# Kernel optimization log

Measured on AMD Instinct MI355X. Metric: run time of the kernel, lower is better.

Reference implementation:

```python
import jax, jax.numpy as jnp
import numpy as np

N_HEAD = 16
D_MODEL = 1024

def setup_inputs() -> dict:
    key = jax.random.key(0)
    ks = jax.random.split(key, 9)
    B, S, D = 8, 1024, D_MODEL
    scale = 1.0 / np.sqrt(D)
    inp = {
        'q': jax.random.normal(ks[0], (B, S, D), jnp.float32),
        'k': jax.random.normal(ks[1], (B, S, D), jnp.float32),
        'v': jax.random.normal(ks[2], (B, S, D), jnp.float32),
        'w_q': jax.random.normal(ks[3], (D, D), jnp.float32) * scale,
        'b_q': jnp.zeros((D,), jnp.float32),
        'w_k': jax.random.normal(ks[4], (D, D), jnp.float32) * scale,
        'b_k': jnp.zeros((D,), jnp.float32),
        'w_v': jax.random.normal(ks[5], (D, D), jnp.float32) * scale,
        'b_v': jnp.zeros((D,), jnp.float32),
    }
    return inp

def reference(q, k, v, w_q, b_q, w_k, b_k, w_v, b_v):
    B, S, D = q.shape
    H = N_HEAD
    dk = D // H
    # QKV projections, split into heads: [B, S, D] -> [B, H, S, dk]
    def proj(x, w, b):
        return (x @ w + b).reshape(B, S, H, dk).transpose(0, 2, 1, 3)
    qh = proj(q, w_q, b_q)
    kh = proj(k, w_k, b_k)
    vh = proj(v, w_v, b_v)
    # scaled dot-product attention (attention matrix materialized as in source)
    scores = jnp.einsum('bhqd,bhkd->bhqk', qh, kh) / jnp.sqrt(jnp.asarray(dk, q.dtype))
    attn = jax.nn.softmax(scores, axis=-1)
    # dropout disabled (eval mode)
    out = jnp.einsum('bhqk,bhkd->bhqd', attn, vh)  # [B, H, S, dk]
    return out.transpose(0, 2, 1, 3).reshape(B, S, D)
```

## Files before the change

kernel.cpp:

```cpp
#include <hip/hip_runtime.h>
#include <hip/hip_bf16.h>

#define BB 8
#define SS 1024
#define DD 1024
#define HH 16
#define DK 64
#define MM (BB*SS)

typedef __attribute__((ext_vector_type(8))) short bf16x8;
typedef __attribute__((ext_vector_type(4))) short bf16x4;
typedef __attribute__((ext_vector_type(4))) float f32x4;
typedef __attribute__((ext_vector_type(4))) int i32x4;

#define QSCALE 0.18033688011112042f

static __device__ __forceinline__ short f2bf(float f) {
    union { float f; unsigned u; } x; x.f = f;
    unsigned r = x.u + 0x7fffu + ((x.u >> 16) & 1u);
    return (short)(r >> 16);
}

#define GLOAD16(g, s) __builtin_amdgcn_global_load_lds( \
    (const __attribute__((address_space(1))) void*)(g), \
    (__attribute__((address_space(3))) void*)(s), 16, 0, 0)

__global__ void wtrans_kernel(const float* __restrict__ w0, const float* __restrict__ w1,
                              const float* __restrict__ w2, short* __restrict__ wt) {
    __shared__ short t[32][33];
    int p = blockIdx.z;
    const float* wsrc = p == 0 ? w0 : (p == 1 ? w1 : w2);
    short* dst = wt + (size_t)p * DD * DD;
    int k0 = blockIdx.y * 32, n0 = blockIdx.x * 32;
    int tx = threadIdx.x & 31, ty = threadIdx.x >> 5;
    #pragma unroll
    for (int i = 0; i < 4; ++i) {
        int k = ty + 8 * i;
        t[k][tx] = f2bf(wsrc[(size_t)(k0 + k) * DD + n0 + tx]);
    }
    __syncthreads();
    #pragma unroll
    for (int i = 0; i < 4; ++i) {
        int n = ty + 8 * i;
        dst[(size_t)(n0 + n) * DD + k0 + tx] = t[tx][n];
    }
}

__global__ void xcast_kernel(const float* __restrict__ xq, const float* __restrict__ xk,
                             const float* __restrict__ xv, short* __restrict__ xbf) {
    int z = blockIdx.y;
    const float* src = z == 0 ? xq : (z == 1 ? xk : xv);
    size_t i = ((size_t)blockIdx.x * 256 + threadIdx.x) * 8;
    f32x4 a = *(const f32x4*)(src + i);
    f32x4 b = *(const f32x4*)(src + i + 4);
    bf16x8 pk;
    pk[0] = f2bf(a[0]); pk[1] = f2bf(a[1]); pk[2] = f2bf(a[2]); pk[3] = f2bf(a[3]);
    pk[4] = f2bf(b[0]); pk[5] = f2bf(b[1]); pk[6] = f2bf(b[2]); pk[7] = f2bf(b[3]);
    *(bf16x8*)(xbf + (size_t)z * MM * DD + i) = pk;
}

#define BM 128
#define BN 128
#define BK 64

template<int ABF16>
__launch_bounds__(256, 3)
__global__ void qkvproj_kernel(const float* __restrict__ xq, const float* __restrict__ xk,
                               const float* __restrict__ xv,
                               const short* __restrict__ xbf,
                               const short* __restrict__ wt,
                               const float* __restrict__ bq, const float* __restrict__ bk,
                               const float* __restrict__ bv,
                               short* __restrict__ qh, short* __restrict__ kh,
                               short* __restrict__ vh) {
    __shared__ short As[BM * 64];
    __shared__ short Bs[BN * 64];
    int lin = blockIdx.x + 8 * (blockIdx.y + 64 * blockIdx.z);
    int sz = (lin & 7) * 192 + (lin >> 3);
    int p = sz >> 9;
    int n0 = (sz & 7) * BN;
    int m0 = ((sz >> 3) & 63) * BM;
    const float* X = p == 0 ? xq : (p == 1 ? xk : xv);
    const short* Wt = wt + (size_t)p * DD * DD;
    const float* bias = p == 0 ? bq : (p == 1 ? bk : bv);
    short* out = p == 0 ? qh : (p == 1 ? kh : vh);
    int t = threadIdx.x;
    int l = t & 63, w = t >> 6;
    int wm = (w >> 1) * 64, wn = (w & 1) * 64;
    int lg = l >> 4, lr = l & 15;
    int rx = lr & 7;

    f32x4 acc[4][4];
    #pragma unroll
    for (int mi = 0; mi < 4; ++mi)
        #pragma unroll
        for (int ni = 0; ni < 4; ++ni) acc[mi][ni] = 0.f;

    for (int k0 = 0; k0 < DD; k0 += BK) {
        __syncthreads();
        if constexpr (ABF16) {
            const short* Xb = xbf + (size_t)p * MM * DD;
            #pragma unroll
            for (int j = 0; j < 4; ++j) {
                int chunk = j * 256 + t;
                int row = chunk >> 3, seg = chunk & 7;
                const short* src = Xb + (size_t)(m0 + row) * DD + k0 + ((seg ^ (row & 7)) * 8);
                GLOAD16(src, &As[(j * 256 + w * 64) * 8]);
            }
        } else {
            #pragma unroll
            for (int i = 0; i < 4; ++i) {
                int c = t + 256 * i;
                int row = c >> 3, seg = c & 7;
                const float* src = X + (size_t)(m0 + row) * DD + k0 + seg * 8;
                f32x4 f0 = *(const f32x4*)(src);
                f32x4 f1 = *(const f32x4*)(src + 4);
                bf16x8 pk;
                pk[0] = f2bf(f0[0]); pk[1] = f2bf(f0[1]); pk[2] = f2bf(f0[2]); pk[3] = f2bf(f0[3]);
                pk[4] = f2bf(f1[0]); pk[5] = f2bf(f1[1]); pk[6] = f2bf(f1[2]); pk[7] = f2bf(f1[3]);
                *(bf16x8*)(&As[row * 64 + ((seg ^ (row & 7)) * 8)]) = pk;
            }
        }
        #pragma unroll
        for (int j = 0; j < 4; ++j) {
            int chunk = j * 256 + t;
            int row = chunk >> 3, seg = chunk & 7;
            const short* src = Wt + (size_t)(n0 + row) * DD + k0 + ((seg ^ (row & 7)) * 8);
            GLOAD16(src, &Bs[(j * 256 + w * 64) * 8]);
        }
        __syncthreads();
        #pragma unroll
        for (int kk = 0; kk < 2; ++kk) {
            bf16x8 a[4], b[4];
            #pragma unroll
            for (int mi = 0; mi < 4; ++mi)
                a[mi] = *(const bf16x8*)(&As[(wm + mi * 16 + lr) * 64 + (((kk * 4 + lg) ^ rx) * 8)]);
            #pragma unroll
            for (int ni = 0; ni < 4; ++ni)
                b[ni] = *(const bf16x8*)(&Bs[(wn + ni * 16 + lr) * 64 + (((kk * 4 + lg) ^ rx) * 8)]);
            #pragma unroll
            for (int mi = 0; mi < 4; ++mi)
                #pragma unroll
                for (int ni = 0; ni < 4; ++ni)
                    acc[mi][ni] = __builtin_amdgcn_mfma_f32_16x16x32_bf16(a[mi], b[ni], acc[mi][ni], 0, 0, 0);
        }
    }
    float osc = (p == 0) ? QSCALE : 1.0f;
    #pragma unroll
    for (int ni = 0; ni < 4; ++ni) {
        int n = n0 + wn + ni * 16 + lr;
        float bvv = bias[n];
        int h = n >> 6, dd = n & 63;
        #pragma unroll
        for (int mi = 0; mi < 4; ++mi) {
            int mbase = m0 + wm + mi * 16 + lg * 4;
            #pragma unroll
            for (int r = 0; r < 4; ++r) {
                int m = mbase + r;
                int b_ = m >> 10, s_ = m & 1023;
                out[(((size_t)(b_ * HH + h) * SS + s_) * DK) + dd] = f2bf((acc[mi][ni][r] + bvv) * osc);
            }
        }
    }
}

__global__ void vtrans_kernel(const short* __restrict__ vh, short* __restrict__ vt) {
    __shared__ short tile[64 * 72];
    int bh = blockIdx.y;
    int s0 = blockIdx.x * 64;
    int t = threadIdx.x;
    #pragma unroll
    for (int i = 0; i < 2; ++i) {
        int c = t + 256 * i;
        int row = c >> 3, dc = (c & 7) * 8;
        *(bf16x8*)&tile[row * 72 + dc] =
            *(const bf16x8*)(vh + ((size_t)bh * SS + s0 + row) * DK + dc);
    }
    __syncthreads();
    #pragma unroll
    for (int i = 0; i < 2; ++i) {
        int c = t + 256 * i;
        int dr = c >> 3, scc = (c & 7) * 8;
        bf16x8 vv;
        #pragma unroll
        for (int j = 0; j < 8; ++j) vv[j] = tile[(scc + j) * 72 + dr];
        *(bf16x8*)(vt + ((size_t)bh * DK + dr) * SS + s0 + scc) = vv;
    }
}


#define SOFTMAX_PV(KT, VT, AQ0, AQ1, MQ, LQ, OO) {                          \
    f32x4 sc[4];                                                            \
    __builtin_amdgcn_s_setprio(1);                                          \
    _Pragma("unroll")                                                       \
    for (int ct = 0; ct < 4; ++ct) {                                        \
        int row = ct * 16 + lr;                                             \
        bf16x8 k0 = *(const bf16x8*)&KT[row * 64 + ((lg ^ sw) * 8)];        \
        bf16x8 k1 = *(const bf16x8*)&KT[row * 64 + (((lg + 4) ^ sw) * 8)];  \
        f32x4 z = 0.f;                                                      \
        z = __builtin_amdgcn_mfma_f32_16x16x32_bf16(k0, AQ0, z, 0, 0, 0);   \
        z = __builtin_amdgcn_mfma_f32_16x16x32_bf16(k1, AQ1, z, 0, 0, 0);   \
        sc[ct] = z;                                                         \
    }                                                                       \
    __builtin_amdgcn_s_setprio(0);                                          \
    float t0 = fmaxf(fmaxf(sc[0][0], sc[0][1]), fmaxf(sc[0][2], sc[0][3])); \
    float t1 = fmaxf(fmaxf(sc[1][0], sc[1][1]), fmaxf(sc[1][2], sc[1][3])); \
    float t2 = fmaxf(fmaxf(sc[2][0], sc[2][1]), fmaxf(sc[2][2], sc[2][3])); \
    float t3 = fmaxf(fmaxf(sc[3][0], sc[3][1]), fmaxf(sc[3][2], sc[3][3])); \
    float tm = fmaxf(fmaxf(t0, t1), fmaxf(t2, t3));                         \
    tm = fmaxf(tm, __shfl_xor(tm, 16, 64));                                 \
    tm = fmaxf(tm, __shfl_xor(tm, 32, 64));                                 \
    if (__any(tm > MQ + 8.0f)) {                                            \
        float mn = fmaxf(MQ, tm);                                           \
        float alpha = exp2f(MQ - mn);                                       \
        MQ = mn; LQ *= alpha;                                               \
        _Pragma("unroll")                                                   \
        for (int r = 0; r < 4; ++r) {                                       \
            float ar = __shfl(alpha, lg * 4 + r, 64);                       \
            OO[0][r] *= ar; OO[1][r] *= ar; OO[2][r] *= ar; OO[3][r] *= ar; \
        }                                                                   \
    }                                                                       \
    float p_[4][4];                                                         \
    _Pragma("unroll")                                                       \
    for (int ct = 0; ct < 4; ++ct) {                                        \
        p_[ct][0] = exp2f(sc[ct][0] - MQ);                                  \
        p_[ct][1] = exp2f(sc[ct][1] - MQ);                                  \
        p_[ct][2] = exp2f(sc[ct][2] - MQ);                                  \
        p_[ct][3] = exp2f(sc[ct][3] - MQ);                                  \
    }                                                                       \
    float rs = ((p_[0][0] + p_[0][1]) + (p_[0][2] + p_[0][3]))              \
             + ((p_[1][0] + p_[1][1]) + (p_[1][2] + p_[1][3]))              \
             + ((p_[2][0] + p_[2][1]) + (p_[2][2] + p_[2][3]))              \
             + ((p_[3][0] + p_[3][1]) + (p_[3][2] + p_[3][3]));             \
    rs += __shfl_xor(rs, 16, 64);                                           \
    rs += __shfl_xor(rs, 32, 64);                                           \
    LQ += rs;                                                               \
    unsigned X00, X01, X10, X11, X20, X21, X30, X31;                        \
    asm("v_cvt_pk_bf16_f32 %0, %1, %2" : "=v"(X00) : "v"(p_[0][0]), "v"(p_[0][1])); \
    asm("v_cvt_pk_bf16_f32 %0, %1, %2" : "=v"(X01) : "v"(p_[0][2]), "v"(p_[0][3])); \
    asm("v_cvt_pk_bf16_f32 %0, %1, %2" : "=v"(X10) : "v"(p_[1][0]), "v"(p_[1][1])); \
    asm("v_cvt_pk_bf16_f32 %0, %1, %2" : "=v"(X11) : "v"(p_[1][2]), "v"(p_[1][3])); \
    asm("v_cvt_pk_bf16_f32 %0, %1, %2" : "=v"(X20) : "v"(p_[2][0]), "v"(p_[2][1])); \
    asm("v_cvt_pk_bf16_f32 %0, %1, %2" : "=v"(X21) : "v"(p_[2][2]), "v"(p_[2][3])); \
    asm("v_cvt_pk_bf16_f32 %0, %1, %2" : "=v"(X30) : "v"(p_[3][0]), "v"(p_[3][1])); \
    asm("v_cvt_pk_bf16_f32 %0, %1, %2" : "=v"(X31) : "v"(p_[3][2]), "v"(p_[3][3])); \
    auto r0 = __builtin_amdgcn_permlane32_swap((int)X00, (int)X10, false, false); \
    auto r1 = __builtin_amdgcn_permlane32_swap((int)X01, (int)X11, false, false); \
    auto r2 = __builtin_amdgcn_permlane32_swap((int)X20, (int)X30, false, false); \
    auto r3 = __builtin_amdgcn_permlane32_swap((int)X21, (int)X31, false, false); \
    i32x4 pa0i = { (int)r0[0], (int)r1[0], (int)r0[1], (int)r1[1] };        \
    i32x4 pa1i = { (int)r2[0], (int)r3[0], (int)r2[1], (int)r3[1] };        \
    bf16x8 pa0 = __builtin_bit_cast(bf16x8, pa0i);                          \
    bf16x8 pa1 = __builtin_bit_cast(bf16x8, pa1i);                          \
    __builtin_amdgcn_s_setprio(1);                                          \
    _Pragma("unroll")                                                       \
    for (int dt = 0; dt < 4; ++dt) {                                        \
        int row = dt * 16 + lr;                                             \
        bf16x8 v0 = *(const bf16x8*)&VT[row * 64 + ((lg ^ sw) * 8)];        \
        bf16x8 v1 = *(const bf16x8*)&VT[row * 64 + (((lg + 4) ^ sw) * 8)];  \
        OO[dt] = __builtin_amdgcn_mfma_f32_16x16x32_bf16(pa0, v0, OO[dt], 0, 0, 0); \
        OO[dt] = __builtin_amdgcn_mfma_f32_16x16x32_bf16(pa1, v1, OO[dt], 0, 0, 0); \
    }                                                                       \
    __builtin_amdgcn_s_setprio(0);                                          \
}

__launch_bounds__(256, 4)
__global__ void attn_kernel(const short* __restrict__ qh, const short* __restrict__ kh,
                            const short* __restrict__ vt, float* __restrict__ out) {
    __shared__ short KBuf[2][64 * 64];
    __shared__ short VBuf[2][64 * 64];
    int lin = blockIdx.y * 8 + blockIdx.x;
    int swz = (lin & 7) * 128 + (lin >> 3);
    int bh = swz >> 3;
    int q0 = (swz & 7) * 128;
    int t = threadIdx.x, l = t & 63, w = t >> 6;
    int lg = l >> 4, lr = l & 15;
    int sw = lr & 7;
    const short* Q  = qh + (size_t)bh * SS * DK;
    const short* Kg = kh + (size_t)bh * SS * DK;
    const short* Vg = vt + (size_t)bh * DK * SS;

    int qrow = q0 + w * 32 + lr;
    bf16x8 aq00 = *(const bf16x8*)(Q + (size_t)qrow * DK + lg * 8);
    bf16x8 aq01 = *(const bf16x8*)(Q + (size_t)qrow * DK + 32 + lg * 8);
    bf16x8 aq10 = *(const bf16x8*)(Q + (size_t)(qrow + 16) * DK + lg * 8);
    bf16x8 aq11 = *(const bf16x8*)(Q + (size_t)(qrow + 16) * DK + 32 + lg * 8);

    float m_q0 = -1e30f, l_q0 = 0.f, m_q1 = -1e30f, l_q1 = 0.f;
    f32x4 o0[4], o1[4];
    #pragma unroll
    for (int dt = 0; dt < 4; ++dt) { o0[dt] = 0.f; o1[dt] = 0.f; }

#define STAGE_KV(kv, b) { \
    _Pragma("unroll") \
    for (int j = 0; j < 2; ++j) { \
        int c = (j * 4 + w) * 64 + l; \
        int row = c >> 3, s = c & 7; \
        int rowg = (row & ~12) | ((row & 4) << 1) | ((row & 8) >> 1); \
        GLOAD16(Kg + (size_t)((kv) + rowg) * DK + ((s ^ (row & 7)) * 8), \
                &KBuf[b][(j * 4 + w) * 512]); \
        GLOAD16(Vg + (size_t)row * SS + (kv) + ((s ^ (row & 7)) * 8), \
                &VBuf[b][(j * 4 + w) * 512]); \
    } }

    STAGE_KV(0, 0);
    __syncthreads();

    for (int tt = 0; tt < 16; ++tt) {
        int cur = tt & 1;
        if (tt < 15) STAGE_KV((tt + 1) * 64, cur ^ 1);
        const short* KT = &KBuf[cur][0];
        const short* VT = &VBuf[cur][0];
        SOFTMAX_PV(KT, VT, aq00, aq01, m_q0, l_q0, o0);
        SOFTMAX_PV(KT, VT, aq10, aq11, m_q1, l_q1, o1);
        __syncthreads();
    }
#undef STAGE_KV

    int b_ = bh >> 4, h_ = bh & 15;
    #pragma unroll
    for (int r = 0; r < 4; ++r) {
        float ls0 = __shfl(l_q0, lg * 4 + r, 64);
        float inv0 = 1.0f / ls0;
        int srow0 = q0 + w * 32 + lg * 4 + r;
        float* op0 = out + ((size_t)(b_ * SS + srow0)) * DD + h_ * DK;
        #pragma unroll
        for (int dt = 0; dt < 4; ++dt)
            op0[dt * 16 + lr] = o0[dt][r] * inv0;
        float ls1 = __shfl(l_q1, lg * 4 + r, 64);
        float inv1 = 1.0f / ls1;
        int srow1 = srow0 + 16;
        float* op1 = out + ((size_t)(b_ * SS + srow1)) * DD + h_ * DK;
        #pragma unroll
        for (int dt = 0; dt < 4; ++dt)
            op1[dt * 16 + lr] = o1[dt][r] * inv1;
    }
}

extern "C" void kernel_launch(void* const* d_in, const int* in_sizes, int n_in,
                              void* d_out, int out_size, void* d_ws, size_t ws_size,
                              hipStream_t stream) {
    const float* q  = (const float*)d_in[0];
    const float* k  = (const float*)d_in[1];
    const float* v  = (const float*)d_in[2];
    const float* wq = (const float*)d_in[3];
    const float* bq = (const float*)d_in[4];
    const float* wk = (const float*)d_in[5];
    const float* bk = (const float*)d_in[6];
    const float* wv = (const float*)d_in[7];
    const float* bv = (const float*)d_in[8];
    float* out = (float*)d_out;

    char* ws = (char*)d_ws;
    const size_t SZ = (size_t)BB * HH * SS * DK * sizeof(short);
    short* Qh = (short*)(ws);
    short* Kh = (short*)(ws + SZ);
    short* Vh = (short*)(ws + 2 * SZ);
    short* Vt = (short*)(ws + 3 * SZ);
    short* Wt = (short*)(ws + 4 * SZ);
    const size_t XOFF = 4 * SZ + 3 * (size_t)DD * DD * sizeof(short);
    short* Xbf = (short*)(ws + XOFF);
    const size_t need = XOFF + 3 * (size_t)MM * DD * sizeof(short);

    wtrans_kernel<<<dim3(32, 32, 3), 256, 0, stream>>>(wq, wk, wv, Wt);
    if (ws_size >= need) {
        xcast_kernel<<<dim3(MM * DD / (256 * 8), 3), 256, 0, stream>>>(q, k, v, Xbf);
        qkvproj_kernel<1><<<dim3(8, 64, 3), 256, 0, stream>>>(q, k, v, Xbf, Wt, bq, bk, bv, Qh, Kh, Vh);
    } else {
        qkvproj_kernel<0><<<dim3(8, 64, 3), 256, 0, stream>>>(q, k, v, nullptr, Wt, bq, bk, bv, Qh, Kh, Vh);
    }
    vtrans_kernel<<<dim3(16, 128), 256, 0, stream>>>(Vh, Vt);
    attn_kernel<<<dim3(8, 128), 256, 0, stream>>>(Qh, Kh, Vt, out);
}
```

Baseline: 155.3 us.

## Fuse fp32 cast into projection loads and compute softmax row sums via MFMA

Drops the separate xcast kernel and its bf16 workspace copy of the inputs. The projection GEMM now always reads fp32 activations and converts them to bf16 in registers before writing to LDS, which saves a full extra read and write pass over the inputs but loses the async global-to-LDS loads for A. In the attention kernel, the softmax row sum is no longer built from VALU adds and shuffles; an extra MFMA against a vector of ones accumulates it, and the max reduction uses v_max3_f32.

After: 164.1 us. 1.06x slower.

```diff
diff --git a/kernel.cpp b/kernel.cpp
--- a/kernel.cpp
+++ b/kernel.cpp
@@ -19,6 +19,12 @@
     union { float f; unsigned u; } x; x.f = f;
     unsigned r = x.u + 0x7fffu + ((x.u >> 16) & 1u);
     return (short)(r >> 16);
+}
+
+static __device__ __forceinline__ float max3f(float a, float b, float c) {
+    float d;
+    asm("v_max3_f32 %0, %1, %2, %3" : "=v"(d) : "v"(a), "v"(b), "v"(c));
+    return d;
 }
 
 #define GLOAD16(g, s) __builtin_amdgcn_global_load_lds( \
@@ -46,28 +52,13 @@
     }
 }
 
-__global__ void xcast_kernel(const float* __restrict__ xq, const float* __restrict__ xk,
-                             const float* __restrict__ xv, short* __restrict__ xbf) {
-    int z = blockIdx.y;
-    const float* src = z == 0 ? xq : (z == 1 ? xk : xv);
-    size_t i = ((size_t)blockIdx.x * 256 + threadIdx.x) * 8;
-    f32x4 a = *(const f32x4*)(src + i);
-    f32x4 b = *(const f32x4*)(src + i + 4);
-    bf16x8 pk;
-    pk[0] = f2bf(a[0]); pk[1] = f2bf(a[1]); pk[2] = f2bf(a[2]); pk[3] = f2bf(a[3]);
-    pk[4] = f2bf(b[0]); pk[5] = f2bf(b[1]); pk[6] = f2bf(b[2]); pk[7] = f2bf(b[3]);
-    *(bf16x8*)(xbf + (size_t)z * MM * DD + i) = pk;
-}
-
 #define BM 128
 #define BN 128
 #define BK 64
 
-template<int ABF16>
 __launch_bounds__(256, 3)
 __global__ void qkvproj_kernel(const float* __restrict__ xq, const float* __restrict__ xk,
                                const float* __restrict__ xv,
-                               const short* __restrict__ xbf,
                                const short* __restrict__ wt,
                                const float* __restrict__ bq, const float* __restrict__ bk,
                                const float* __restrict__ bv,
@@ -98,28 +89,17 @@
 
     for (int k0 = 0; k0 < DD; k0 += BK) {
         __syncthreads();
-        if constexpr (ABF16) {
-            const short* Xb = xbf + (size_t)p * MM * DD;
-            #pragma unroll
-            for (int j = 0; j < 4; ++j) {
-                int chunk = j * 256 + t;
-                int row = chunk >> 3, seg = chunk & 7;
-                const short* src = Xb + (size_t)(m0 + row) * DD + k0 + ((seg ^ (row & 7)) * 8);
-                GLOAD16(src, &As[(j * 256 + w * 64) * 8]);
-            }
-        } else {
-            #pragma unroll
-            for (int i = 0; i < 4; ++i) {
-                int c = t + 256 * i;
-                int row = c >> 3, seg = c & 7;
-                const float* src = X + (size_t)(m0 + row) * DD + k0 + seg * 8;
-                f32x4 f0 = *(const f32x4*)(src);
-                f32x4 f1 = *(const f32x4*)(src + 4);
-                bf16x8 pk;
-                pk[0] = f2bf(f0[0]); pk[1] = f2bf(f0[1]); pk[2] = f2bf(f0[2]); pk[3] = f2bf(f0[3]);
-                pk[4] = f2bf(f1[0]); pk[5] = f2bf(f1[1]); pk[6] = f2bf(f1[2]); pk[7] = f2bf(f1[3]);
-                *(bf16x8*)(&As[row * 64 + ((seg ^ (row & 7)) * 8)]) = pk;
-            }
+        #pragma unroll
+        for (int i = 0; i < 4; ++i) {
+            int c = t + 256 * i;
+            int row = c >> 3, seg = c & 7;
+            const float* src = X + (size_t)(m0 + row) * DD + k0 + seg * 8;
+            f32x4 f0 = *(const f32x4*)(src);
+            f32x4 f1 = *(const f32x4*)(src + 4);
+            bf16x8 pk;
+            pk[0] = f2bf(f0[0]); pk[1] = f2bf(f0[1]); pk[2] = f2bf(f0[2]); pk[3] = f2bf(f0[3]);
+            pk[4] = f2bf(f1[0]); pk[5] = f2bf(f1[1]); pk[6] = f2bf(f1[2]); pk[7] = f2bf(f1[3]);
+            *(bf16x8*)(&As[row * 64 + ((seg ^ (row & 7)) * 8)]) = pk;
         }
         #pragma unroll
         for (int j = 0; j < 4; ++j) {
@@ -189,7 +169,7 @@
 }
 
 
-#define SOFTMAX_PV(KT, VT, AQ0, AQ1, MQ, LQ, OO) {                          \
+#define SOFTMAX_PV(KT, VT, AQ0, AQ1, MQ, OO, OS) {                          \
     f32x4 sc[4];                                                            \
     __builtin_amdgcn_s_setprio(1);                                          \
     _Pragma("unroll")                                                       \
@@ -203,21 +183,25 @@
         sc[ct] = z;                                                         \
     }                                                                       \
     __builtin_amdgcn_s_setprio(0);                                          \
-    float t0 = fmaxf(fmaxf(sc[0][0], sc[0][1]), fmaxf(sc[0][2], sc[0][3])); \
-    float t1 = fmaxf(fmaxf(sc[1][0], sc[1][1]), fmaxf(sc[1][2], sc[1][3])); \
-    float t2 = fmaxf(fmaxf(sc[2][0], sc[2][1]), fmaxf(sc[2][2], sc[2][3])); \
-    float t3 = fmaxf(fmaxf(sc[3][0], sc[3][1]), fmaxf(sc[3][2], sc[3][3])); \
-    float tm = fmaxf(fmaxf(t0, t1), fmaxf(t2, t3));                         \
+    float ta = max3f(sc[0][0], sc[0][1], sc[0][2]);                         \
+    float tb = max3f(sc[0][3], sc[1][0], sc[1][1]);                         \
+    float tc = max3f(sc[1][2], sc[1][3], sc[2][0]);                         \
+    float td = max3f(sc[2][1], sc[2][2], sc[2][3]);                         \
+    float te = max3f(sc[3][0], sc[3][1], sc[3][2]);                         \
+    float tf = max3f(ta, tb, tc);                                           \
+    float tg = max3f(td, te, sc[3][3]);                                     \
+    float tm = fmaxf(tf, tg);                                               \
     tm = fmaxf(tm, __shfl_xor(tm, 16, 64));                                 \
     tm = fmaxf(tm, __shfl_xor(tm, 32, 64));                                 \
     if (__any(tm > MQ + 8.0f)) {                                            \
         float mn = fmaxf(MQ, tm);                                           \
         float alpha = exp2f(MQ - mn);                                       \
-        MQ = mn; LQ *= alpha;                                               \
+        MQ = mn;                                                            \
         _Pragma("unroll")                                                   \
         for (int r = 0; r < 4; ++r) {                                       \
             float ar = __shfl(alpha, lg * 4 + r, 64);                       \
             OO[0][r] *= ar; OO[1][r] *= ar; OO[2][r] *= ar; OO[3][r] *= ar; \
+            OS[r] *= ar;                                                    \
         }                                                                   \
     }                                                                       \
     float p_[4][4];                                                         \
@@ -228,13 +212,6 @@
         p_[ct][2] = exp2f(sc[ct][2] - MQ);                                  \
         p_[ct][3] = exp2f(sc[ct][3] - MQ);                                  \
     }                                                                       \
-    float rs = ((p_[0][0] + p_[0][1]) + (p_[0][2] + p_[0][3]))              \
-             + ((p_[1][0] + p_[1][1]) + (p_[1][2] + p_[1][3]))              \
-             + ((p_[2][0] + p_[2][1]) + (p_[2][2] + p_[2][3]))              \
-             + ((p_[3][0] + p_[3][1]) + (p_[3][2] + p_[3][3]));             \
-    rs += __shfl_xor(rs, 16, 64);                                           \
-    rs += __shfl_xor(rs, 32, 64);                                           \
-    LQ += rs;                                                               \
     unsigned X00, X01, X10, X11, X20, X21, X30, X31;                        \
     asm("v_cvt_pk_bf16_f32 %0, %1, %2" : "=v"(X00) : "v"(p_[0][0]), "v"(p_[0][1])); \
     asm("v_cvt_pk_bf16_f32 %0, %1, %2" : "=v"(X01) : "v"(p_[0][2]), "v"(p_[0][3])); \
@@ -261,6 +238,8 @@
         OO[dt] = __builtin_amdgcn_mfma_f32_16x16x32_bf16(pa0, v0, OO[dt], 0, 0, 0); \
         OO[dt] = __builtin_amdgcn_mfma_f32_16x16x32_bf16(pa1, v1, OO[dt], 0, 0, 0); \
     }                                                                       \
+    OS = __builtin_amdgcn_mfma_f32_16x16x32_bf16(pa0, vones, OS, 0, 0, 0);  \
+    OS = __builtin_amdgcn_mfma_f32_16x16x32_bf16(pa1, vones, OS, 0, 0, 0);  \
     __builtin_amdgcn_s_setprio(0);                                          \
 }
 
@@ -280,16 +259,21 @@
     const short* Kg = kh + (size_t)bh * SS * DK;
     const short* Vg = vt + (size_t)bh * DK * SS;
 
+    bf16x8 vones;
+    #pragma unroll
+    for (int i = 0; i < 8; ++i) vones[i] = (short)0x3F80;
+
     int qrow = q0 + w * 32 + lr;
     bf16x8 aq00 = *(const bf16x8*)(Q + (size_t)qrow * DK + lg * 8);
     bf16x8 aq01 = *(const bf16x8*)(Q + (size_t)qrow * DK + 32 + lg * 8);
     bf16x8 aq10 = *(const bf16x8*)(Q + (size_t)(qrow + 16) * DK + lg * 8);
     bf16x8 aq11 = *(const bf16x8*)(Q + (size_t)(qrow + 16) * DK + 32 + lg * 8);
 
-    float m_q0 = -1e30f, l_q0 = 0.f, m_q1 = -1e30f, l_q1 = 0.f;
-    f32x4 o0[4], o1[4];
+    float m_q0 = -1e30f, m_q1 = -1e30f;
+    f32x4 o0[4], o1[4], os0, os1;
     #pragma unroll
     for (int dt = 0; dt < 4; ++dt) { o0[dt] = 0.f; o1[dt] = 0.f; }
+    os0 = 0.f; os1 = 0.f;
 
 #define STAGE_KV(kv, b) { \
     _Pragma("unroll") \
@@ -311,8 +295,8 @@
         if (tt < 15) STAGE_KV((tt + 1) * 64, cur ^ 1);
         const short* KT = &KBuf[cur][0];
         const short* VT = &VBuf[cur][0];
-        SOFTMAX_PV(KT, VT, aq00, aq01, m_q0, l_q0, o0);
-        SOFTMAX_PV(KT, VT, aq10, aq11, m_q1, l_q1, o1);
+        SOFTMAX_PV(KT, VT, aq00, aq01, m_q0, o0, os0);
+        SOFTMAX_PV(KT, VT, aq10, aq11, m_q1, o1, os1);
         __syncthreads();
     }
 #undef STAGE_KV
@@ -320,15 +304,13 @@
     int b_ = bh >> 4, h_ = bh & 15;
     #pragma unroll
     for (int r = 0; r < 4; ++r) {
-        float ls0 = __shfl(l_q0, lg * 4 + r, 64);
-        float inv0 = 1.0f / ls0;
+        float inv0 = 1.0f / os0[r];
         int srow0 = q0 + w * 32 + lg * 4 + r;
         float* op0 = out + ((size_t)(b_ * SS + srow0)) * DD + h_ * DK;
         #pragma unroll
         for (int dt = 0; dt < 4; ++dt)
             op0[dt * 16 + lr] = o0[dt][r] * inv0;
-        float ls1 = __shfl(l_q1, lg * 4 + r, 64);
-        float inv1 = 1.0f / ls1;
+        float inv1 = 1.0f / os1[r];
         int srow1 = srow0 + 16;
         float* op1 = out + ((size_t)(b_ * SS + srow1)) * DD + h_ * DK;
         #pragma unroll
@@ -358,17 +340,9 @@
     short* Vh = (short*)(ws + 2 * SZ);
     short* Vt = (short*)(ws + 3 * SZ);
     short* Wt = (short*)(ws + 4 * SZ);
-    const size_t XOFF = 4 * SZ + 3 * (size_t)DD * DD * sizeof(short);
-    short* Xbf = (short*)(ws + XOFF);
-    const size_t need = XOFF + 3 * (size_t)MM * DD * sizeof(short);
 
     wtrans_kernel<<<dim3(32, 32, 3), 256, 0, stream>>>(wq, wk, wv, Wt);
-    if (ws_size >= need) {
-        xcast_kernel<<<dim3(MM * DD / (256 * 8), 3), 256, 0, stream>>>(q, k, v, Xbf);
-        qkvproj_kernel<1><<<dim3(8, 64, 3), 256, 0, stream>>>(q, k, v, Xbf, Wt, bq, bk, bv, Qh, Kh, Vh);
-    } else {
-        qkvproj_kernel<0><<<dim3(8, 64, 3), 256, 0, stream>>>(q, k, v, nullptr, Wt, bq, bk, bv, Qh, Kh, Vh);
-    }
+    qkvproj_kernel<<<dim3(8, 64, 3), 256, 0, stream>>>(q, k, v, Wt, bq, bk, bv, Qh, Kh, Vh);
     vtrans_kernel<<<dim3(16, 128), 256, 0, stream>>>(Vh, Vt);
     attn_kernel<<<dim3(8, 128), 256, 0, stream>>>(Qh, Kh, Vt, out);
 }
```
